# Kernel optimization log

Measured on AMD Instinct MI355X. Metric: run time of the kernel, lower is better.

## Reference

```python
import jax, jax.numpy as jnp
import numpy as np

BASE = 10000.0

def _rope_neox(x, positions, head_dim):
    # x: [B, S, n_heads, head_dim]; positions: [B, S] int
    half = head_dim // 2
    inv_freq = 1.0 / (BASE ** (jnp.arange(0, head_dim, 2, dtype=jnp.float32) / head_dim))  # [half]
    freqs = positions.astype(jnp.float32)[..., None] * inv_freq  # [B, S, half]
    cos = jnp.cos(freqs)[:, :, None, :]  # [B, S, 1, half]
    sin = jnp.sin(freqs)[:, :, None, :]
    x1, x2 = x[..., :half], x[..., half:]
    return jnp.concatenate([x1 * cos - x2 * sin, x2 * cos + x1 * sin], axis=-1)

def setup_inputs() -> dict:
    key = jax.random.key(0)
    k1, k2, k3 = jax.random.split(key, 3)
    B, S, H = 1, 2048, 4096
    hidden_states = jax.random.normal(k1, (B, S, H), dtype=jnp.float32)
    position_ids = jnp.broadcast_to(jnp.arange(S, dtype=jnp.int32), (B, S))
    W_qkv = jax.random.normal(k2, (H, 3 * H), dtype=jnp.float32) * (H ** -0.5)
    W_o = jax.random.normal(k3, (H, H), dtype=jnp.float32) * (H ** -0.5)
    return {"hidden_states": hidden_states, "position_ids": position_ids, "W_qkv": W_qkv, "W_o": W_o}

def reference(hidden_states, position_ids, W_qkv, W_o):
    B, S, H = hidden_states.shape
    n_heads = 32
    head_dim = H // n_heads
    qkv = hidden_states @ W_qkv  # [B, S, 3H]
    q, k, v = jnp.split(qkv, 3, axis=-1)
    q = q.reshape(B, S, n_heads, head_dim)
    k = k.reshape(B, S, n_heads, head_dim)
    v = v.reshape(B, S, n_heads, head_dim)
    q = _rope_neox(q, position_ids, head_dim)
    k = _rope_neox(k, position_ids, head_dim)
    # causal SDPA (past_key_value=None -> is_causal=True)
    scale = 1.0 / jnp.sqrt(jnp.float32(head_dim))
    scores = jnp.einsum('bqhd,bkhd->bhqk', q, k) * scale  # [B, nH, S, S]
    causal = jnp.tril(jnp.ones((S, S), dtype=bool))
    scores = jnp.where(causal, scores, jnp.finfo(scores.dtype).min)
    probs = jax.nn.softmax(scores, axis=-1)
    attn = jnp.einsum('bhqk,bkhd->bqhd', probs, v).reshape(B, S, H)
    return attn @ W_o
```

## Files before the change

kernel.cpp:

```cpp
#include <hip/hip_runtime.h>
#include <hip/hip_bf16.h>
#include <math.h>

#define SEQ   2048
#define HID   4096
#define NHEAD 32
#define HD    128
#define QKVN  12288

typedef __bf16 bf16;
typedef __bf16 bf16x8 __attribute__((ext_vector_type(8)));
typedef __bf16 bf16x4 __attribute__((ext_vector_type(4)));
typedef float  f32x4  __attribute__((ext_vector_type(4)));

#define AS1 __attribute__((address_space(1)))
#define AS3 __attribute__((address_space(3)))

__device__ __forceinline__ void gload16(const void* g, void* l) {
    __builtin_amdgcn_global_load_lds((const AS1 void*)g, (AS3 void*)l, 16, 0, 0);
}

__device__ __forceinline__ unsigned short bbits(bf16 b) {
    union { bf16 b; unsigned short u; } x; x.b = b; return x.u;
}

template<int OB>
__global__ __launch_bounds__(512, 2) void gemm2p(const bf16* __restrict__ A,
                                                 const bf16* __restrict__ Bt,
                                                 void* __restrict__ Cv,
                                                 int M, int N, int K, int gx) {
    __shared__ __attribute__((aligned(16))) char lds[98304];
    const int tid  = threadIdx.x;
    const int l    = tid & 63;
    const int wave = tid >> 6;
    const int wr   = wave >> 2;
    const int wc   = wave & 3;
    const int lh   = l >> 4;
    const int ll   = l & 15;

    const int id   = blockIdx.x;
    const int xcd  = id & 7;
    const int slot = id >> 3;
    const int bx   = xcd * (gx >> 3) + (slot >> 3);
    const int by   = slot & 7;
    const int brow = by * 256, bcol = bx * 128;

    f32x4 acc[2][4][2];
    #pragma unroll
    for (int m = 0; m < 2; ++m)
        #pragma unroll
        for (int f = 0; f < 4; ++f)
            #pragma unroll
            for (int g = 0; g < 2; ++g) acc[m][f][g] = (f32x4){0.f, 0.f, 0.f, 0.f};

    const int trow = tid >> 3, tslot = tid & 7;
    const int srcs = (tslot ^ (trow & 7)) * 16;
    const size_t rowb = (size_t)K * 2;
    const char* pA[2][2]; const char* pB[2];
    #pragma unroll
    for (int h = 0; h < 2; ++h)
        #pragma unroll
        for (int i = 0; i < 2; ++i)
            pA[h][i] = (const char*)A + (size_t)(brow + h*128 + i*64 + trow) * rowb + srcs;
    #pragma unroll
    for (int i = 0; i < 2; ++i)
        pB[i] = (const char*)Bt + (size_t)(bcol + i*64 + trow) * rowb + srcs;

#define SA(buf, h) do { \
        gload16(pA[h][0], lds + (buf)*32768 + (h)*16384 + tid*16); \
        gload16(pA[h][1], lds + (buf)*32768 + (h)*16384 + 8192 + tid*16); \
        pA[h][0] += 128; pA[h][1] += 128; \
    } while (0)
#define SB(buf) do { \
        gload16(pB[0], lds + 65536 + (buf)*16384 + tid*16); \
        gload16(pB[1], lds + 65536 + (buf)*16384 + 8192 + tid*16); \
        pB[0] += 128; pB[1] += 128; \
    } while (0)

    const int sw0 = ((0 + lh) ^ (ll & 7)) << 4;
    const int sw1 = ((4 + lh) ^ (ll & 7)) << 4;

#define PHASE(Xb, mh, STAGE_STMT, WAITSTR) do { \
        const char* LA_ = lds + (Xb)*32768 + (mh)*16384 + (wr*64 + ll)*128; \
        const char* LB_ = lds + 65536 + (Xb)*16384 + (wc*32 + ll)*128; \
        bf16x8 af_[4][2], bv_[2][2]; \
        _Pragma("unroll") \
        for (int f_ = 0; f_ < 4; ++f_) { \
            af_[f_][0] = *(const bf16x8*)(LA_ + f_*2048 + sw0); \
            af_[f_][1] = *(const bf16x8*)(LA_ + f_*2048 + sw1); \
        } \
        _Pragma("unroll") \
        for (int g_ = 0; g_ < 2; ++g_) { \
            bv_[g_][0] = *(const bf16x8*)(LB_ + g_*2048 + sw0); \
            bv_[g_][1] = *(const bf16x8*)(LB_ + g_*2048 + sw1); \
        } \
        STAGE_STMT; \
        asm volatile(WAITSTR ::: "memory"); \
        __builtin_amdgcn_s_barrier(); \
        asm volatile("s_waitcnt lgkmcnt(0)" ::: "memory"); \
        __builtin_amdgcn_sched_barrier(0); \
        __builtin_amdgcn_s_setprio(1); \
        _Pragma("unroll") \
        for (int f_ = 0; f_ < 4; ++f_) \
            _Pragma("unroll") \
            for (int g_ = 0; g_ < 2; ++g_) { \
                acc[mh][f_][g_] = __builtin_amdgcn_mfma_f32_16x16x32_bf16( \
                    af_[f_][0], bv_[g_][0], acc[mh][f_][g_], 0, 0, 0); \
                acc[mh][f_][g_] = __builtin_amdgcn_mfma_f32_16x16x32_bf16( \
                    af_[f_][1], bv_[g_][1], acc[mh][f_][g_], 0, 0, 0); \
            } \
        __builtin_amdgcn_s_setprio(0); \
        __builtin_amdgcn_s_barrier(); \
    } while (0)

    SA(0, 0); SB(0); SA(0, 1); SA(1, 0);
    asm volatile("s_waitcnt vmcnt(4)" ::: "memory");
    __builtin_amdgcn_s_barrier();

    const int NT = K >> 6;
    for (int u = 0; u < NT - 2; ++u) {
        const int X = u & 1, Y = X ^ 1;
        PHASE(X, 0, SB(Y), "s_waitcnt vmcnt(4)");
        PHASE(X, 1, { SA(Y, 1); SA(X, 0); }, "s_waitcnt vmcnt(4)");
    }
    {
        const int X = (NT - 2) & 1, Y = X ^ 1;
        PHASE(X, 0, SB(Y), "s_waitcnt vmcnt(4)");
        PHASE(X, 1, SA(Y, 1), "s_waitcnt vmcnt(2)");
    }
    {
        const int X = (NT - 1) & 1;
        PHASE(X, 0, ((void)0), "s_waitcnt vmcnt(0)");
        PHASE(X, 1, ((void)0), "s_nop 0");
    }
#undef PHASE
#undef SA
#undef SB

    __syncthreads();
    float* ep = (float*)lds + wave * 2304;
    const int cq = l & 3;
    #pragma unroll
    for (int mh = 0; mh < 2; ++mh) {
        #pragma unroll
        for (int f = 0; f < 4; ++f)
            #pragma unroll
            for (int g = 0; g < 2; ++g)
                #pragma unroll
                for (int j = 0; j < 4; ++j)
                    ep[(f*16 + lh*4 + j) * 36 + g*16 + ll] = acc[mh][f][g][j];
        #pragma unroll
        for (int it = 0; it < 4; ++it) {
            int r2 = it * 16 + (l >> 2);
            const float* src = ep + r2 * 36 + cq * 8;
            size_t grow = (size_t)(brow + mh*128 + wr*64 + r2);
            int gcol = bcol + wc*32 + cq*8;
            if (OB == 0) {
                float* dst = (float*)Cv + grow * N + gcol;
                *(f32x4*)dst       = *(const f32x4*)src;
                *(f32x4*)(dst + 4) = *(const f32x4*)(src + 4);
            } else {
                bf16x8 o;
                #pragma unroll
                for (int jj = 0; jj < 8; ++jj) o[jj] = (bf16)src[jj];
                *(bf16x8*)((bf16*)Cv + grow * N + gcol) = o;
            }
        }
    }
}

__global__ __launch_bounds__(256) void cast_flat(const float* __restrict__ in,
                                                 bf16* __restrict__ out, int n8) {
    int i = blockIdx.x * 256 + threadIdx.x;
    if (i >= n8) return;
    float4 a = ((const float4*)in)[2 * i];
    float4 b = ((const float4*)in)[2 * i + 1];
    bf16x8 o = {(bf16)a.x, (bf16)a.y, (bf16)a.z, (bf16)a.w,
                (bf16)b.x, (bf16)b.y, (bf16)b.z, (bf16)b.w};
    *(bf16x8*)(out + (size_t)i * 8) = o;
}

__global__ __launch_bounds__(256) void cast_transpose(const float* __restrict__ in,
                                                      bf16* __restrict__ out, int R, int C) {
    __shared__ float t[64][65];
    const int r0 = blockIdx.y * 64, c0 = blockIdx.x * 64;
    #pragma unroll
    for (int i = 0; i < 4; ++i) {
        int idx = i * 256 + threadIdx.x;
        int rr = idx >> 4, c4 = (idx & 15) * 4;
        float4 v = *(const float4*)&in[(size_t)(r0 + rr) * C + c0 + c4];
        t[rr][c4] = v.x; t[rr][c4 + 1] = v.y; t[rr][c4 + 2] = v.z; t[rr][c4 + 3] = v.w;
    }
    __syncthreads();
    #pragma unroll
    for (int i = 0; i < 2; ++i) {
        int idx = i * 256 + threadIdx.x;
        int rr = idx >> 3, c8 = (idx & 7) * 8;
        bf16x8 o;
        #pragma unroll
        for (int j = 0; j < 8; ++j) o[j] = (bf16)t[c8 + j][rr];
        *(bf16x8*)&out[(size_t)(c0 + rr) * R + r0 + c8] = o;
    }
}

__global__ __launch_bounds__(256) void rope_table(const int* __restrict__ pos_ids,
                                                  float2* __restrict__ tab) {
    int id = blockIdx.x * 256 + threadIdx.x;
    int s = id >> 6, d = id & 63;
    float pos = (float)pos_ids[s];
    float inv = expf(-9.210340371976184f * ((float)d * (1.0f / 64.0f)));
    float sn, cs;
    sincosf(pos * inv, &sn, &cs);
    tab[id] = make_float2(cs, sn);
}

__global__ __launch_bounds__(256) void rope_repack(const bf16* __restrict__ qkv,
                                                   const float2* __restrict__ tab,
                                                   bf16* __restrict__ Qb,
                                                   bf16* __restrict__ Kb) {
    int id = blockIdx.x * 256 + threadIdx.x;
    const int d4 = (id & 15) * 4;
    const int h  = (id >> 4) & (NHEAD - 1);
    const int s  = id >> 9;

    float2 tr[4];
    #pragma unroll
    for (int i = 0; i < 4; ++i) tr[i] = tab[s * 64 + d4 + i];

    const bf16* row = qkv + (size_t)s * QKVN;
    {
        bf16x4 lo = *(const bf16x4*)(row + h * HD + d4);
        bf16x4 hi = *(const bf16x4*)(row + h * HD + 64 + d4);
        bf16x4 olo, ohi;
        #pragma unroll
        for (int i = 0; i < 4; ++i) {
            float x1 = (float)lo[i], x2 = (float)hi[i];
            olo[i] = (bf16)(x1 * tr[i].x - x2 * tr[i].y);
            ohi[i] = (bf16)(x2 * tr[i].x + x1 * tr[i].y);
        }
        bf16* qo = Qb + ((size_t)h * SEQ + s) * HD;
        *(bf16x4*)(qo + d4) = olo;
        *(bf16x4*)(qo + 64 + d4) = ohi;
    }
    {
        bf16x4 lo = *(const bf16x4*)(row + HID + h * HD + d4);
        bf16x4 hi = *(const bf16x4*)(row + HID + h * HD + 64 + d4);
        bf16x4 olo, ohi;
        #pragma unroll
        for (int i = 0; i < 4; ++i) {
            float x1 = (float)lo[i], x2 = (float)hi[i];
            olo[i] = (bf16)(x1 * tr[i].x - x2 * tr[i].y);
            ohi[i] = (bf16)(x2 * tr[i].x + x1 * tr[i].y);
        }
        bf16* ko = Kb + ((size_t)h * SEQ + s) * HD;
        *(bf16x4*)(ko + d4) = olo;
        *(bf16x4*)(ko + 64 + d4) = ohi;
    }
}

__global__ __launch_bounds__(256) void v_transpose(const bf16* __restrict__ qkv,
                                                   bf16* __restrict__ Vt) {
    __shared__ bf16 t[64][130];
    const int h = blockIdx.y, s0 = blockIdx.x * 64;
    #pragma unroll
    for (int i = 0; i < 4; ++i) {
        int idx = i * 256 + threadIdx.x;
        int ss = idx >> 4, c8 = (idx & 15) * 8;
        bf16x8 v = *(const bf16x8*)&qkv[(size_t)(s0 + ss) * QKVN + 2 * HID + h * HD + c8];
        #pragma unroll
        for (int j = 0; j < 8; ++j) t[ss][c8 + j] = v[j];
    }
    __syncthreads();
    #pragma unroll
    for (int i = 0; i < 4; ++i) {
        int idx = i * 256 + threadIdx.x;
        int dd = idx >> 3, s8 = (idx & 7) * 8;
        bf16x8 o;
        #pragma unroll
        for (int j = 0; j < 8; ++j) o[j] = t[s8 + j][dd];
        *(bf16x8*)&Vt[((size_t)h * HD + dd) * SEQ + s0 + s8] = o;
    }
}

__global__ __launch_bounds__(256) void attn_mfma(const bf16* __restrict__ Qb,
                                                 const bf16* __restrict__ Kb,
                                                 const bf16* __restrict__ Vt,
                                                 bf16* __restrict__ attn) {
    __shared__ __attribute__((aligned(16))) char Ka[2][16384];
    __shared__ __attribute__((aligned(16))) char Va[2][16384];
    __shared__ __attribute__((aligned(16))) char Ps[4 * 2048];
    const int tid  = threadIdx.x, l = tid & 63, wave = tid >> 6;
    const int head = blockIdx.x;
    const int qb   = gridDim.y - 1 - blockIdx.y;
    const int q0   = qb * 64;
    const int qw   = q0 + wave * 16;
    const float scale = 0.08838834764831845f;

    bf16x8 qf[4];
    const bf16* Qg = Qb + ((size_t)head * SEQ + qw + (l & 15)) * HD;
    #pragma unroll
    for (int kc = 0; kc < 4; ++kc) qf[kc] = *(const bf16x8*)(Qg + kc * 32 + (l >> 4) * 8);

    f32x4 o[8];
    #pragma unroll
    for (int i = 0; i < 8; ++i) o[i] = (f32x4){0.f, 0.f, 0.f, 0.f};
    float mrun = -1e30f, lrun = 0.f;
    const int qrow  = qw + (l & 15);
    const int ntile = qb + 1;

    const char* Kg = (const char*)(Kb + (size_t)head * SEQ * HD);
    const char* Vg = (const char*)(Vt + (size_t)head * HD * SEQ);
    char* Pw = Ps + wave * 2048;

#define ASTAGE(b, t0) do { \
        const int kv0_ = (t0) * 64; \
        _Pragma("unroll") \
        for (int i = 0; i < 4; ++i) { \
            int c = i * 256 + tid; \
            int rk_ = c >> 4, slk_ = c & 15; \
            gload16(Kg + (size_t)(kv0_ + rk_) * 256 + ((slk_ * 16) ^ ((rk_ & 15) << 4)), \
                    Ka[b] + (size_t)(i * 256 + (tid & 192)) * 16); \
            int rv_ = c >> 3, slv_ = c & 7; \
            gload16(Vg + (size_t)rv_ * (SEQ * 2) + (size_t)kv0_ * 2 + ((slv_ * 16) ^ ((rv_ & 7) << 4)), \
                    Va[b] + (size_t)(i * 256 + (tid & 192)) * 16); \
        } \
    } while (0)

    ASTAGE(0, 0);
    asm volatile("s_waitcnt vmcnt(0)" ::: "memory");
    __builtin_amdgcn_s_barrier();

    for (int t = 0; t < ntile; ++t) {
        const int cur = t & 1;
        const int kv0 = t * 64;
        if (t + 1 < ntile) ASTAGE(cur ^ 1, t + 1);

        f32x4 st[4];
        __builtin_amdgcn_s_setprio(1);
        #pragma unroll
        for (int mf = 0; mf < 4; ++mf) {
            f32x4 s = (f32x4){0.f, 0.f, 0.f, 0.f};
            #pragma unroll
            for (int kc = 0; kc < 4; ++kc) {
                int rk = mf * 16 + (l & 15);
                bf16x8 a = *(const bf16x8*)(Ka[cur] + rk * 256 +
                              ((kc * 64 + (l >> 4) * 16) ^ ((rk & 15) << 4)));
                s = __builtin_amdgcn_mfma_f32_16x16x32_bf16(a, qf[kc], s, 0, 0, 0);
            }
            st[mf] = s;
        }
        __builtin_amdgcn_s_setprio(0);

        float pm = -1e30f;
        #pragma unroll
        for (int mf = 0; mf < 4; ++mf)
            #pragma unroll
            for (int j = 0; j < 4; ++j) {
                int kv = kv0 + mf * 16 + (l >> 4) * 4 + j;
                float v = (kv <= qrow) ? st[mf][j] * scale : -1e30f;
                st[mf][j] = v;
                pm = fmaxf(pm, v);
            }
        pm = fmaxf(pm, __shfl_xor(pm, 16));
        pm = fmaxf(pm, __shfl_xor(pm, 32));
        float mn   = fmaxf(mrun, pm);
        float corr = __expf(mrun - mn);
        float ls = 0.f;
        #pragma unroll
        for (int mf = 0; mf < 4; ++mf)
            #pragma unroll
            for (int j = 0; j < 4; ++j) {
                float p = __expf(st[mf][j] - mn);
                st[mf][j] = p;
                ls += p;
            }
        ls += __shfl_xor(ls, 16);
        ls += __shfl_xor(ls, 32);
        lrun = lrun * corr + ls;
        mrun = mn;

        f32x4 cv;
        #pragma unroll
        for (int r = 0; r < 4; ++r) cv[r] = __shfl(corr, (l >> 4) * 4 + r, 64);
        #pragma unroll
        for (int nf = 0; nf < 8; ++nf) o[nf] *= cv;

        #pragma unroll
        for (int mf = 0; mf < 4; ++mf)
            #pragma unroll
            for (int r = 0; r < 4; r += 2) {
                int kv = mf * 16 + (l >> 4) * 4 + r;
                unsigned pk = (unsigned)bbits((bf16)st[mf][r]) |
                              ((unsigned)bbits((bf16)st[mf][r + 1]) << 16);
                *(unsigned*)(Pw + (l & 15) * 128 + ((kv * 2) ^ ((l & 15 & 7) << 4))) = pk;
            }

        __builtin_amdgcn_s_setprio(1);
        #pragma unroll
        for (int kc = 0; kc < 2; ++kc) {
            bf16x8 pa = *(const bf16x8*)(Pw + (l & 15) * 128 +
                           ((kc * 64 + (l >> 4) * 16) ^ ((l & 7) << 4)));
            #pragma unroll
            for (int nf = 0; nf < 8; ++nf) {
                int dr = nf * 16 + (l & 15);
                bf16x8 vb = *(const bf16x8*)(Va[cur] + dr * 128 +
                               ((kc * 64 + (l >> 4) * 16) ^ ((dr & 7) << 4)));
                o[nf] = __builtin_amdgcn_mfma_f32_16x16x32_bf16(pa, vb, o[nf], 0, 0, 0);
            }
        }
        __builtin_amdgcn_s_setprio(0);

        asm volatile("s_waitcnt vmcnt(0) lgkmcnt(0)" ::: "memory");
        __builtin_amdgcn_s_barrier();
    }
#undef ASTAGE

    float il = 1.0f / lrun;
    f32x4 iv;
    #pragma unroll
    for (int r = 0; r < 4; ++r) iv[r] = __shfl(il, (l >> 4) * 4 + r, 64);
    #pragma unroll
    for (int nf = 0; nf < 8; ++nf)
        #pragma unroll
        for (int r = 0; r < 4; ++r) {
            int row = qw + (l >> 4) * 4 + r;
            attn[(size_t)row * HID + head * HD + nf * 16 + (l & 15)] = (bf16)(o[nf][r] * iv[r]);
        }
}

extern "C" void kernel_launch(void* const* d_in, const int* in_sizes, int n_in,
                              void* d_out, int out_size, void* d_ws, size_t ws_size,
                              hipStream_t stream) {
    const float* hidden  = (const float*)d_in[0];
    const int*   pos_ids = (const int*)d_in[1];
    const float* W_qkv   = (const float*)d_in[2];
    const float* W_o     = (const float*)d_in[3];
    float*       out     = (float*)d_out;
    char*        ws      = (char*)d_ws;

    bf16*   Wqkv_t   = (bf16*)(ws);
    bf16*   qkv_b    = (bf16*)(ws + 100663296);
    bf16*   hidden_b = (bf16*)(ws + 150994944);
    float2* tab      = (float2*)(ws + 150994944);
    bf16* Qb     = (bf16*)(ws);
    bf16* Kb     = (bf16*)(ws + 16777216);
    bf16* Vtb    = (bf16*)(ws + 33554432);
    bf16* attn_b = (bf16*)(ws + 50331648);
    bf16* Wo_t   = (bf16*)(ws + 67108864);

    cast_flat<<<SEQ * HID / 8 / 256, 256, 0, stream>>>(hidden, hidden_b, SEQ * HID / 8);
    cast_transpose<<<dim3(QKVN / 64, HID / 64), 256, 0, stream>>>(W_qkv, Wqkv_t, HID, QKVN);
    gemm2p<1><<<(QKVN / 128) * (SEQ / 256), 512, 0, stream>>>(hidden_b, Wqkv_t, qkv_b,
                                                              SEQ, QKVN, HID, QKVN / 128);
    rope_table<<<SEQ * 64 / 256, 256, 0, stream>>>(pos_ids, tab);
    rope_repack<<<SEQ * NHEAD * 16 / 256, 256, 0, stream>>>(qkv_b, tab, Qb, Kb);
    v_transpose<<<dim3(SEQ / 64, NHEAD), 256, 0, stream>>>(qkv_b, Vtb);
    cast_transpose<<<dim3(HID / 64, HID / 64), 256, 0, stream>>>(W_o, Wo_t, HID, HID);
    attn_mfma<<<dim3(NHEAD, SEQ / 64), 256, 0, stream>>>(Qb, Kb, Vtb, attn_b);
    gemm2p<0><<<(HID / 128) * (SEQ / 256), 512, 0, stream>>>(attn_b, Wo_t, out,
                                                             SEQ, HID, HID, HID / 128);
}
```

Measured before the change: 463.8 us.

## Add 256x256-tile bf16 GEMM with quarter-phased pipeline for QKV projection

Adds a new GEMM kernel with 256x256 output tiles and a 128KB double-buffered LDS pipeline. It splits each K-step into four MFMA quarter phases that interleave LDS fragment loads with async global-to-LDS loads. This raises arithmetic intensity per loaded byte for the large QKV projection but limits occupancy to one block per CU. It also drops the XCD-aware block remapping from the existing gemm2p kernel, which may hurt L2 locality for the output projection.

```diff
diff --git a/kernel.cpp b/kernel.cpp
--- a/kernel.cpp
+++ b/kernel.cpp
@@ -24,11 +24,155 @@
     union { bf16 b; unsigned short u; } x; x.b = b; return x.u;
 }
 
+__global__ __launch_bounds__(512) __attribute__((amdgpu_waves_per_eu(2, 2)))
+void gemm256(const bf16* __restrict__ A, const bf16* __restrict__ Bt,
+             bf16* __restrict__ C, int M, int N, int K) {
+    __shared__ __attribute__((aligned(16))) char lds[131072];
+    const int tid  = threadIdx.x;
+    const int l    = tid & 63;
+    const int wave = tid >> 6;
+    const int wr   = wave >> 2;
+    const int wc   = wave & 3;
+    const int lh   = l >> 4;
+    const int ll   = l & 15;
+    const int by   = blockIdx.x & 7, bx = blockIdx.x >> 3;
+    const int brow = by * 256, bcol = bx * 256;
+
+    f32x4 acc[4][4][2];
+    #pragma unroll
+    for (int q = 0; q < 4; ++q)
+        #pragma unroll
+        for (int f = 0; f < 4; ++f)
+            #pragma unroll
+            for (int g = 0; g < 2; ++g) acc[q][f][g] = (f32x4){0.f, 0.f, 0.f, 0.f};
+
+    const int trow = tid >> 3, tslot = tid & 7;
+    const int srcs = (tslot ^ (trow & 7)) * 16;
+    const size_t rowb = (size_t)K * 2;
+    const char* pA[2][2]; const char* pB[2][2];
+    #pragma unroll
+    for (int h = 0; h < 2; ++h)
+        #pragma unroll
+        for (int i = 0; i < 2; ++i) {
+            pA[h][i] = (const char*)A  + (size_t)(brow + h*128 + i*64 + trow) * rowb + srcs;
+            pB[h][i] = (const char*)Bt + (size_t)(bcol + h*128 + i*64 + trow) * rowb + srcs;
+        }
+
+#define SA(buf, h) do { \
+        gload16(pA[h][0], lds + (buf)*65536 + (h)*16384 + tid*16); \
+        gload16(pA[h][1], lds + (buf)*65536 + (h)*16384 + 8192 + tid*16); \
+        pA[h][0] += 128; pA[h][1] += 128; \
+    } while (0)
+#define SB(buf, h) do { \
+        gload16(pB[h][0], lds + (buf)*65536 + 32768 + (h)*16384 + tid*16); \
+        gload16(pB[h][1], lds + (buf)*65536 + 32768 + (h)*16384 + 8192 + tid*16); \
+        pB[h][0] += 128; pB[h][1] += 128; \
+    } while (0)
+
+    const int sw0 = ((0 + lh) ^ (ll & 7)) << 4;
+    const int sw1 = ((4 + lh) ^ (ll & 7)) << 4;
+
+    bf16x8 af[4][2], bv0[2][2], bv1[2][2];
+
+#define LOADA(Xb, mh) do { \
+        const char* LA_ = lds + (Xb)*65536 + (mh)*16384 + (wr*64 + ll)*128; \
+        _Pragma("unroll") \
+        for (int f_ = 0; f_ < 4; ++f_) { \
+            af[f_][0] = *(const bf16x8*)(LA_ + f_*2048 + sw0); \
+            af[f_][1] = *(const bf16x8*)(LA_ + f_*2048 + sw1); \
+        } \
+    } while (0)
+#define LOADB(Xb, nh, bvv) do { \
+        const char* LB_ = lds + (Xb)*65536 + 32768 + (nh)*16384 + (wc*32 + ll)*128; \
+        _Pragma("unroll") \
+        for (int g_ = 0; g_ < 2; ++g_) { \
+            bvv[g_][0] = *(const bf16x8*)(LB_ + g_*2048 + sw0); \
+            bvv[g_][1] = *(const bf16x8*)(LB_ + g_*2048 + sw1); \
+        } \
+    } while (0)
+#define FENCE_MMA(WAITSTR, q, bvv) do { \
+        asm volatile(WAITSTR ::: "memory"); \
+        __builtin_amdgcn_s_barrier(); \
+        asm volatile("s_waitcnt lgkmcnt(0)" ::: "memory"); \
+        __builtin_amdgcn_sched_barrier(0); \
+        __builtin_amdgcn_s_setprio(1); \
+        _Pragma("unroll") \
+        for (int f_ = 0; f_ < 4; ++f_) \
+            _Pragma("unroll") \
+            for (int g_ = 0; g_ < 2; ++g_) { \
+                acc[q][f_][g_] = __builtin_amdgcn_mfma_f32_16x16x32_bf16( \
+                    af[f_][0], bvv[g_][0], acc[q][f_][g_], 0, 0, 0); \
+                acc[q][f_][g_] = __builtin_amdgcn_mfma_f32_16x16x32_bf16( \
+                    af[f_][1], bvv[g_][1], acc[q][f_][g_], 0, 0, 0); \
+            } \
+        __builtin_amdgcn_s_setprio(0); \
+        __builtin_amdgcn_s_barrier(); \
+    } while (0)
+
+    SA(0, 0); SB(0, 0); SB(0, 1); SA(0, 1); SA(1, 0); SB(1, 0);
+    asm volatile("s_waitcnt vmcnt(8)" ::: "memory");
+    __builtin_amdgcn_s_barrier();
+
+    const int NT = K >> 6;
+    for (int u = 0; u < NT - 1; ++u) {
+        const int X = u & 1, Y = X ^ 1;
+        LOADA(X, 0); LOADB(X, 0, bv0); SB(Y, 1);
+        FENCE_MMA("s_waitcnt vmcnt(8)", 0, bv0);
+        LOADB(X, 1, bv1); SA(Y, 1);
+        FENCE_MMA("s_waitcnt vmcnt(8)", 1, bv1);
+        LOADA(X, 1);
+        if (u < NT - 2) { SA(X, 0); }
+        FENCE_MMA("s_waitcnt vmcnt(8)", 2, bv0);
+        if (u < NT - 2) { SB(X, 0); }
+        FENCE_MMA("s_waitcnt vmcnt(8)", 3, bv1);
+    }
+    {
+        const int X = (NT - 1) & 1;
+        LOADA(X, 0); LOADB(X, 0, bv0);
+        FENCE_MMA("s_waitcnt vmcnt(4)", 0, bv0);
+        LOADB(X, 1, bv1);
+        FENCE_MMA("s_waitcnt vmcnt(2)", 1, bv1);
+        LOADA(X, 1);
+        FENCE_MMA("s_waitcnt vmcnt(0)", 2, bv0);
+        FENCE_MMA("s_nop 0", 3, bv1);
+    }
+#undef FENCE_MMA
+#undef LOADA
+#undef LOADB
+#undef SA
+#undef SB
+
+    __syncthreads();
+    float* ep = (float*)lds + wave * 2304;
+    const int c8 = (l & 3) * 8;
+    #pragma unroll
+    for (int q = 0; q < 4; ++q) {
+        const int mh = q >> 1, nh = q & 1;
+        #pragma unroll
+        for (int f = 0; f < 4; ++f)
+            #pragma unroll
+            for (int g = 0; g < 2; ++g)
+                #pragma unroll
+                for (int j = 0; j < 4; ++j)
+                    ep[(f*16 + lh*4 + j) * 36 + g*16 + ll] = acc[q][f][g][j];
+        #pragma unroll
+        for (int it = 0; it < 4; ++it) {
+            int r2 = it * 16 + (l >> 2);
+            const float* src = ep + r2 * 36 + c8;
+            bf16x8 o;
+            #pragma unroll
+            for (int j = 0; j < 8; ++j) o[j] = (bf16)src[j];
+            size_t grow = (size_t)(brow + mh*128 + wr*64 + r2);
+            *(bf16x8*)(C + grow * N + bcol + nh*128 + wc*32 + c8) = o;
+        }
+    }
+}
+
 template<int OB>
 __global__ __launch_bounds__(512, 2) void gemm2p(const bf16* __restrict__ A,
                                                  const bf16* __restrict__ Bt,
                                                  void* __restrict__ Cv,
-                                                 int M, int N, int K, int gx) {
+                                                 int M, int N, int K) {
     __shared__ __attribute__((aligned(16))) char lds[98304];
     const int tid  = threadIdx.x;
     const int l    = tid & 63;
@@ -38,11 +182,8 @@
     const int lh   = l >> 4;
     const int ll   = l & 15;
 
-    const int id   = blockIdx.x;
-    const int xcd  = id & 7;
-    const int slot = id >> 3;
-    const int bx   = xcd * (gx >> 3) + (slot >> 3);
-    const int by   = slot & 7;
+    const int by   = blockIdx.x & 7;
+    const int bx   = blockIdx.x >> 3;
     const int brow = by * 256, bcol = bx * 128;
 
     f32x4 acc[2][4][2];
@@ -450,13 +591,13 @@
 
     cast_flat<<<SEQ * HID / 8 / 256, 256, 0, stream>>>(hidden, hidden_b, SEQ * HID / 8);
     cast_transpose<<<dim3(QKVN / 64, HID / 64), 256, 0, stream>>>(W_qkv, Wqkv_t, HID, QKVN);
-    gemm2p<1><<<(QKVN / 128) * (SEQ / 256), 512, 0, stream>>>(hidden_b, Wqkv_t, qkv_b,
-                                                              SEQ, QKVN, HID, QKVN / 128);
+    gemm256<<<(QKVN / 256) * (SEQ / 256), 512, 0, stream>>>(hidden_b, Wqkv_t, qkv_b,
+                                                            SEQ, QKVN, HID);
     rope_table<<<SEQ * 64 / 256, 256, 0, stream>>>(pos_ids, tab);
     rope_repack<<<SEQ * NHEAD * 16 / 256, 256, 0, stream>>>(qkv_b, tab, Qb, Kb);
     v_transpose<<<dim3(SEQ / 64, NHEAD), 256, 0, stream>>>(qkv_b, Vtb);
     cast_transpose<<<dim3(HID / 64, HID / 64), 256, 0, stream>>>(W_o, Wo_t, HID, HID);
     attn_mfma<<<dim3(NHEAD, SEQ / 64), 256, 0, stream>>>(Qb, Kb, Vtb, attn_b);
     gemm2p<0><<<(HID / 128) * (SEQ / 256), 512, 0, stream>>>(attn_b, Wo_t, out,
-                                                             SEQ, HID, HID, HID / 128);
-}
+                                                             SEQ, HID, HID);
+}
```

Result: no change. 458.9 us (-1.0%).
